# Performance work log

Hardware: AMD Instinct MI355X
Metric: run time of the kernel (lower is better)

The kernel has to match this reference:

```python
import jax, jax.numpy as jnp
import numpy as np

N_NODES = 50000
N_EDGES = 800000
HID = 64


def fake_quant_w(w):
    # symmetric per-tensor int8 fake quantization (num_bits=8)
    s = jnp.maximum(jnp.max(jnp.abs(w)) / 127.0, 1e-8)
    q = jnp.clip(jnp.round(w / s), -127.0, 127.0) * s
    return w + jax.lax.stop_gradient(q - w)


def layer_norm(x, g, b, eps=1e-5):
    mu = jnp.mean(x, axis=-1, keepdims=True)
    var = jnp.var(x, axis=-1, keepdims=True)
    return (x - mu) * jax.lax.rsqrt(var + eps) * g + b


def pointnet_conv(x, pos, src, dst, W, n_nodes):
    # message: cat([x_j, pos_j - pos_i]) @ W_q^T, max-aggregated at i (dst)
    rel = pos[src] - pos[dst]                       # [E, 3]
    feat = jnp.concatenate([x[src], rel], axis=-1)  # [E, C+3]
    msg = feat @ fake_quant_w(W).T                  # [E, 64]
    h = jax.ops.segment_max(msg, dst, num_segments=n_nodes)
    return jnp.where(jnp.isfinite(h), h, 0.0)       # empty segments -> 0


def setup_inputs() -> dict:
    key = jax.random.key(0)
    ks = jax.random.split(key, 16)
    d = {}
    d["x"] = jax.random.normal(ks[0], (N_NODES, 1), jnp.float32)
    d["pos"] = jax.random.normal(ks[1], (N_NODES, 3), jnp.float32)
    d["edge_index"] = jax.random.randint(ks[2], (2, N_EDGES), 0, N_NODES, jnp.int32)
    sc = 0.02
    d["W0"] = jax.random.normal(ks[3], (HID, 1 + 3), jnp.float32) * sc
    d["Ws"] = jax.random.normal(ks[4], (4, HID, HID + 3), jnp.float32) * sc
    d["ln_g"] = jnp.ones((5, HID), jnp.float32)
    d["ln_b"] = jnp.zeros((5, HID), jnp.float32)
    d["mlp_w1"] = jax.random.normal(ks[5], (128, 320), jnp.float32) * sc
    d["mlp_b1"] = jnp.zeros((128,), jnp.float32)
    d["mlp_w2"] = jax.random.normal(ks[6], (128, 128), jnp.float32) * sc
    d["mlp_b2"] = jnp.zeros((128,), jnp.float32)
    d["mlp_w3"] = jax.random.normal(ks[7], (64, 128), jnp.float32) * sc
    d["mlp_b3"] = jnp.zeros((64,), jnp.float32)
    d["mlp_w4"] = jax.random.normal(ks[8], (2, 64), jnp.float32) * sc
    d["mlp_b4"] = jnp.zeros((2,), jnp.float32)
    d["scale"] = jnp.ones((2,), jnp.float32)
    return d


def reference(x, pos, edge_index, W0, Ws, ln_g, ln_b,
              mlp_w1, mlp_b1, mlp_w2, mlp_b2, mlp_w3, mlp_b3, mlp_w4, mlp_b4,
              scale):
    src, dst = edge_index[0], edge_index[1]
    n = x.shape[0]
    embeddings = []
    h = x
    for i in range(5):
        W = W0 if i == 0 else Ws[i - 1]
        h = pointnet_conv(h, pos, src, dst, W, n)
        h = layer_norm(h, ln_g[i], ln_b[i])
        h = jax.nn.relu(h)
        embeddings.append(h)
    z = jnp.concatenate(embeddings, axis=-1)  # [N, 320]
    z = layer_norm(z, jnp.ones((z.shape[-1],), z.dtype), jnp.zeros((z.shape[-1],), z.dtype))
    z = jax.nn.relu(z @ mlp_w1.T + mlp_b1)
    z = jax.nn.relu(z @ mlp_w2.T + mlp_b2)
    z = jax.nn.relu(z @ mlp_w3.T + mlp_b3)
    flow = (z @ mlp_w4.T + mlp_b4) * scale
    return flow
```

## Files before the change

### kernel.cpp

```cpp
#include <hip/hip_runtime.h>
#include <hip/hip_bf16.h>

#define N_NODES 50000
#define N_EDGES 800000
#define NBLK 196

__device__ __forceinline__ float bf2f(unsigned short u) {
    union { unsigned int i; float f; } c; c.i = ((unsigned int)u) << 16; return c.f;
}
__device__ __forceinline__ unsigned short f2bf(float f) {
    union { float f; unsigned int u; } c; c.f = f;
    unsigned int u = c.u;
    u += 0x7fffu + ((u >> 16) & 1u);
    return (unsigned short)(u >> 16);
}
__device__ __forceinline__ float ldin(const void* p, long i, int f32) {
    return f32 ? ((const float*)p)[i] : bf2f(((const unsigned short*)p)[i]);
}
__device__ __forceinline__ float wsum(float v) {
#pragma unroll
    for (int m = 32; m; m >>= 1) v += __shfl_xor(v, m, 64);
    return v;
}

__global__ void probe_kernel(const unsigned short* __restrict__ lng, int* __restrict__ flag) {
    if (threadIdx.x == 0 && blockIdx.x == 0)
        flag[0] = (lng[0] == 0x3F80 && lng[1] == 0x3F80) ? 0 : 1;
}

__global__ __launch_bounds__(256) void hist_kernel(const int* __restrict__ ei, int* __restrict__ deg) {
    int e = blockIdx.x * 256 + threadIdx.x;
    if (e < N_EDGES) atomicAdd(&deg[ei[N_EDGES + e]], 1);
}

__global__ __launch_bounds__(256) void bsum_kernel(const int* __restrict__ deg,
                                                   int* __restrict__ bsum) {
    __shared__ int wt[4];
    const int t = threadIdx.x, lane = t & 63, wid = t >> 6;
    const int i = blockIdx.x * 256 + t;
    int v = (i < N_NODES) ? deg[i] : 0;
    int r = v;
#pragma unroll
    for (int m = 32; m; m >>= 1) r += __shfl_xor(r, m, 64);
    if (lane == 0) wt[wid] = r;
    __syncthreads();
    if (t == 0) bsum[blockIdx.x] = wt[0] + wt[1] + wt[2] + wt[3];
}

__global__ __launch_bounds__(256) void boff_kernel(const int* __restrict__ bsum,
                                                   int* __restrict__ boff) {
    __shared__ int wt[4];
    const int t = threadIdx.x, lane = t & 63, wid = t >> 6;
    int v = (t < NBLK) ? bsum[t] : 0;
    int inc = v;
#pragma unroll
    for (int off = 1; off < 64; off <<= 1) {
        int u = __shfl_up(inc, off, 64);
        if (lane >= off) inc += u;
    }
    if (lane == 63) wt[wid] = inc;
    __syncthreads();
    int woff = 0;
    for (int w = 0; w < wid; ++w) woff += wt[w];
    if (t < NBLK) boff[t] = inc - v + woff;
}

__global__ __launch_bounds__(256) void scanout_kernel(const int* __restrict__ deg,
                                                      const int* __restrict__ boff,
                                                      int* __restrict__ rowptr,
                                                      int* __restrict__ cursor) {
    __shared__ int wt[4];
    const int t = threadIdx.x, lane = t & 63, wid = t >> 6;
    const int i = blockIdx.x * 256 + t;
    int v = (i < N_NODES) ? deg[i] : 0;
    int inc = v;
#pragma unroll
    for (int off = 1; off < 64; off <<= 1) {
        int u = __shfl_up(inc, off, 64);
        if (lane >= off) inc += u;
    }
    if (lane == 63) wt[wid] = inc;
    __syncthreads();
    int woff = 0;
    for (int w = 0; w < wid; ++w) woff += wt[w];
    int excl = inc - v + woff + boff[blockIdx.x];
    if (i < N_NODES) {
        rowptr[i] = excl;
        cursor[i] = excl;
        if (i == N_NODES - 1) rowptr[N_NODES] = excl + v;
    }
}

__global__ __launch_bounds__(256) void scatter_kernel(const int* __restrict__ ei,
                                                      int* __restrict__ cursor,
                                                      int* __restrict__ csr_src) {
    int e = blockIdx.x * 256 + threadIdx.x;
    if (e < N_EDGES) {
        int src = ei[e];
        int dst = ei[N_EDGES + e];
        int p = atomicAdd(&cursor[dst], 1);
        csr_src[p] = src;
    }
}

__global__ __launch_bounds__(256) void quant_kernel(const void* __restrict__ W0,
                                                    const void* __restrict__ Ws,
                                                    float* __restrict__ Wc0,
                                                    float* __restrict__ Wc,
                                                    float* __restrict__ Wr,
                                                    const int* __restrict__ flagp) {
    const int f32 = *flagp;
    int layer = blockIdx.x;
    const void* src = (layer == 0) ? W0 : Ws;
    long sbase = (layer == 0) ? 0 : (long)(layer - 1) * 4288;
    float* dstc = (layer == 0) ? Wc0 : Wc + (size_t)(layer - 1) * 4352;
    float* dstr = (layer == 0) ? nullptr : Wr + (size_t)(layer - 1) * 4352;
    int Ki = (layer == 0) ? 4 : 67;
    int n = 64 * Ki;
    __shared__ float red[256];
    float amax = 0.0f;
    for (int i = threadIdx.x; i < n; i += 256) amax = fmaxf(amax, fabsf(ldin(src, sbase + i, f32)));
    red[threadIdx.x] = amax;
    __syncthreads();
    for (int s = 128; s > 0; s >>= 1) {
        if (threadIdx.x < s) red[threadIdx.x] = fmaxf(red[threadIdx.x], red[threadIdx.x + s]);
        __syncthreads();
    }
    float sc = fmaxf(red[0] / 127.0f, 1e-8f);
    for (int i = threadIdx.x; i < n; i += 256) {
        float w = ldin(src, sbase + i, f32);
        float q = rintf(w / sc);
        q = fminf(fmaxf(q, -127.0f), 127.0f);
        float v = q * sc;
        int o = i / Ki, k = i % Ki;
        dstc[(size_t)k * 64 + o] = v;
        if (dstr) dstr[(size_t)o * 68 + k] = v;
    }
}

__global__ __launch_bounds__(256) void wcvt_kernel(const void* __restrict__ w1,
                                                   const void* __restrict__ w2,
                                                   const void* __restrict__ w3,
                                                   float* __restrict__ Wm,
                                                   const int* __restrict__ flagp) {
    const int f32 = *flagp;
    const int i = blockIdx.x * 256 + threadIdx.x;
    if (i < 40960) Wm[i] = ldin(w1, i, f32);
    else if (i < 57344) Wm[i] = ldin(w2, i - 40960, f32);
    else if (i < 65536) Wm[i] = ldin(w3, i - 57344, f32);
}

__global__ __launch_bounds__(256) void u0_kernel(const void* __restrict__ x,
                                                 const void* __restrict__ pos,
                                                 const float* __restrict__ Wc0,
                                                 float* __restrict__ u,
                                                 const int* __restrict__ flagp) {
    const int f32 = *flagp;
    const int n = blockIdx.x * 256 + threadIdx.x;
    if (n >= N_NODES) return;
    const float xv = ldin(x, n, f32);
    const float p0 = ldin(pos, 3L * n + 0, f32);
    const float p1 = ldin(pos, 3L * n + 1, f32);
    const float p2 = ldin(pos, 3L * n + 2, f32);
    float4* up = reinterpret_cast<float4*>(u + (size_t)n * 64);
#pragma unroll
    for (int q = 0; q < 16; ++q) {
        const float4 w0 = *reinterpret_cast<const float4*>(Wc0 + 0 * 64 + 4 * q);
        const float4 w1 = *reinterpret_cast<const float4*>(Wc0 + 1 * 64 + 4 * q);
        const float4 w2 = *reinterpret_cast<const float4*>(Wc0 + 2 * 64 + 4 * q);
        const float4 w3 = *reinterpret_cast<const float4*>(Wc0 + 3 * 64 + 4 * q);
        float4 o;
        o.x = fmaf(p2, w3.x, fmaf(p1, w2.x, fmaf(p0, w1.x, xv * w0.x)));
        o.y = fmaf(p2, w3.y, fmaf(p1, w2.y, fmaf(p0, w1.y, xv * w0.y)));
        o.z = fmaf(p2, w3.z, fmaf(p1, w2.z, fmaf(p0, w1.z, xv * w0.z)));
        o.w = fmaf(p2, w3.w, fmaf(p1, w2.w, fmaf(p0, w1.w, xv * w0.w)));
        up[q] = o;
    }
}

__global__ __launch_bounds__(256) void agg_kernel(const float* __restrict__ u,
                                                  const void* __restrict__ pos,
                                                  const int* __restrict__ rowptr,
                                                  const int* __restrict__ csr,
                                                  const float* __restrict__ WcV, int vrow,
                                                  const void* __restrict__ lng,
                                                  const void* __restrict__ lnb,
                                                  int lnoff,
                                                  float* __restrict__ z, int out_off,
                                                  const int* __restrict__ flagp) {
    const int f32 = *flagp;
    const int lane = threadIdx.x & 63;
    const int n = __builtin_amdgcn_readfirstlane((blockIdx.x * 256 + threadIdx.x) >> 6);
    if (n >= N_NODES) return;
    const int e0 = rowptr[n], e1 = rowptr[n + 1];
    float acc = -INFINITY;
    int e = e0;
    for (; e + 8 <= e1; e += 8) {
        const float a0 = u[(size_t)csr[e + 0] * 64 + lane];
        const float a1 = u[(size_t)csr[e + 1] * 64 + lane];
        const float a2 = u[(size_t)csr[e + 2] * 64 + lane];
        const float a3 = u[(size_t)csr[e + 3] * 64 + lane];
        const float a4 = u[(size_t)csr[e + 4] * 64 + lane];
        const float a5 = u[(size_t)csr[e + 5] * 64 + lane];
        const float a6 = u[(size_t)csr[e + 6] * 64 + lane];
        const float a7 = u[(size_t)csr[e + 7] * 64 + lane];
        const float m0 = fmaxf(fmaxf(a0, a1), fmaxf(a2, a3));
        const float m1 = fmaxf(fmaxf(a4, a5), fmaxf(a6, a7));
        acc = fmaxf(acc, fmaxf(m0, m1));
    }
    for (; e < e1; ++e)
        acc = fmaxf(acc, u[(size_t)csr[e] * 64 + lane]);
    const float p0 = ldin(pos, 3L * n + 0, f32);
    const float p1 = ldin(pos, 3L * n + 1, f32);
    const float p2 = ldin(pos, 3L * n + 2, f32);
    const float v = fmaf(p2, WcV[(size_t)(vrow + 2) * 64 + lane],
                    fmaf(p1, WcV[(size_t)(vrow + 1) * 64 + lane],
                         p0 * WcV[(size_t)(vrow + 0) * 64 + lane]));
    float h = acc - v;
    if (!isfinite(h)) h = 0.0f;
    const float g = ldin(lng, lnoff + lane, f32);
    const float bb = ldin(lnb, lnoff + lane, f32);
    const float mu = wsum(h) * (1.0f / 64.0f);
    const float dd = h - mu;
    const float var = wsum(dd * dd) * (1.0f / 64.0f);
    float y = dd * rsqrtf(var + 1e-5f) * g + bb;
    y = fmaxf(y, 0.0f);
    z[(size_t)n * 320 + out_off + lane] = y;
}

__global__ __launch_bounds__(256) void un_kernel(const float* __restrict__ z, int in_off,
                                                 const float* __restrict__ Wr,
                                                 const void* __restrict__ pos,
                                                 float* __restrict__ un,
                                                 const int* __restrict__ flagp) {
    __shared__ float At[16][68];
    __shared__ float Wt[16][68];
    const int f32 = *flagp;
    const int tid = threadIdx.x;
    const int bn = blockIdx.x * 64;
    const int o_base = (tid & 15) * 4;
    const int n_base = (tid >> 4) * 4;
    const int sr = tid >> 2;
    const int kq = (tid & 3) * 4;
    float acc[4][4] = {};
    float4 av = make_float4(0.f, 0.f, 0.f, 0.f);
    if (bn + sr < N_NODES)
        av = *reinterpret_cast<const float4*>(z + (size_t)(bn + sr) * 320 + in_off + kq);
    float4 wv = *reinterpret_cast<const float4*>(Wr + (size_t)sr * 68 + kq);
    for (int kk = 0; kk < 64; kk += 16) {
        __syncthreads();
        At[kq + 0][sr] = av.x; At[kq + 1][sr] = av.y; At[kq + 2][sr] = av.z; At[kq + 3][sr] = av.w;
        Wt[kq + 0][sr] = wv.x; Wt[kq + 1][sr] = wv.y; Wt[kq + 2][sr] = wv.z; Wt[kq + 3][sr] = wv.w;
        __syncthreads();
        if (kk + 16 < 64) {
            av = make_float4(0.f, 0.f, 0.f, 0.f);
            if (bn + sr < N_NODES)
                av = *reinterpret_cast<const float4*>(z + (size_t)(bn + sr) * 320 + in_off + kk + 16 + kq);
            wv = *reinterpret_cast<const float4*>(Wr + (size_t)sr * 68 + kk + 16 + kq);
        }
#pragma unroll
        for (int k = 0; k < 16; ++k) {
            const float4 a4 = *reinterpret_cast<const float4*>(&At[k][n_base]);
            const float4 w4 = *reinterpret_cast<const float4*>(&Wt[k][o_base]);
            const float a[4] = { a4.x, a4.y, a4.z, a4.w };
            const float ww[4] = { w4.x, w4.y, w4.z, w4.w };
#pragma unroll
            for (int i = 0; i < 4; ++i)
#pragma unroll
                for (int j = 0; j < 4; ++j)
                    acc[i][j] = fmaf(a[i], ww[j], acc[i][j]);
        }
    }
    float wp[3][4];
#pragma unroll
    for (int c = 0; c < 3; ++c)
#pragma unroll
        for (int j = 0; j < 4; ++j)
            wp[c][j] = Wr[(size_t)(o_base + j) * 68 + 64 + c];
#pragma unroll
    for (int i = 0; i < 4; ++i) {
        const int n = bn + n_base + i;
        if (n < N_NODES) {
            const float p0 = ldin(pos, 3L * n + 0, f32);
            const float p1 = ldin(pos, 3L * n + 1, f32);
            const float p2 = ldin(pos, 3L * n + 2, f32);
#pragma unroll
            for (int j = 0; j < 4; ++j)
                un[(size_t)n * 64 + o_base + j] =
                    fmaf(p2, wp[2][j], fmaf(p1, wp[1][j], fmaf(p0, wp[0][j], acc[i][j])));
        }
    }
}

__global__ __launch_bounds__(256) void lnz_kernel(float* __restrict__ z) {
    const int lane = threadIdx.x & 63;
    const int gw = (blockIdx.x * blockDim.x + threadIdx.x) >> 6;
    const int nw = (gridDim.x * blockDim.x) >> 6;
    for (int nidx = gw; nidx < N_NODES; nidx += nw) {
        float v[5];
        float s = 0.f;
#pragma unroll
        for (int j = 0; j < 5; ++j) {
            v[j] = z[(size_t)nidx * 320 + j * 64 + lane];
            s += v[j];
        }
        float mu = wsum(s) * (1.0f / 320.0f);
        float q = 0.f;
#pragma unroll
        for (int j = 0; j < 5; ++j) { float d = v[j] - mu; q = fmaf(d, d, q); }
        float var = wsum(q) * (1.0f / 320.0f);
        float rs = rsqrtf(var + 1e-5f);
#pragma unroll
        for (int j = 0; j < 5; ++j) z[(size_t)nidx * 320 + j * 64 + lane] = (v[j] - mu) * rs;
    }
}

__global__ __launch_bounds__(256) void gemm_kernel(const float* __restrict__ A,
                                                   const float* __restrict__ W,
                                                   const void* __restrict__ bias,
                                                   float* __restrict__ C,
                                                   int Ki, int Ko,
                                                   const int* __restrict__ flagp) {
    __shared__ float At[16][68];
    __shared__ float Wt[16][68];
    const int f32 = *flagp;
    const int tid = threadIdx.x;
    const int bn = blockIdx.x * 64;
    const int bo = blockIdx.y * 64;
    const int o_base = (tid & 15) * 4;
    const int n_base = (tid >> 4) * 4;
    const int sr = tid >> 2;
    const int kq = (tid & 3) * 4;
    float acc[4][4] = {};
    float4 av = make_float4(0.f, 0.f, 0.f, 0.f);
    if (bn + sr < N_NODES)
        av = *reinterpret_cast<const float4*>(A + (size_t)(bn + sr) * Ki + kq);
    float4 wv = *reinterpret_cast<const float4*>(W + (size_t)(bo + sr) * Ki + kq);
    for (int kk = 0; kk < Ki; kk += 16) {
        __syncthreads();
        At[kq + 0][sr] = av.x; At[kq + 1][sr] = av.y; At[kq + 2][sr] = av.z; At[kq + 3][sr] = av.w;
        Wt[kq + 0][sr] = wv.x; Wt[kq + 1][sr] = wv.y; Wt[kq + 2][sr] = wv.z; Wt[kq + 3][sr] = wv.w;
        __syncthreads();
        if (kk + 16 < Ki) {
            av = make_float4(0.f, 0.f, 0.f, 0.f);
            if (bn + sr < N_NODES)
                av = *reinterpret_cast<const float4*>(A + (size_t)(bn + sr) * Ki + kk + 16 + kq);
            wv = *reinterpret_cast<const float4*>(W + (size_t)(bo + sr) * Ki + kk + 16 + kq);
        }
#pragma unroll
        for (int k = 0; k < 16; ++k) {
            const float4 a4 = *reinterpret_cast<const float4*>(&At[k][n_base]);
            const float4 w4 = *reinterpret_cast<const float4*>(&Wt[k][o_base]);
            const float a[4] = { a4.x, a4.y, a4.z, a4.w };
            const float ww[4] = { w4.x, w4.y, w4.z, w4.w };
#pragma unroll
            for (int i = 0; i < 4; ++i)
#pragma unroll
                for (int j = 0; j < 4; ++j)
                    acc[i][j] = fmaf(a[i], ww[j], acc[i][j]);
        }
    }
    float bj[4];
#pragma unroll
    for (int j = 0; j < 4; ++j) bj[j] = ldin(bias, bo + o_base + j, f32);
#pragma unroll
    for (int i = 0; i < 4; ++i) {
        int n = bn + n_base + i;
        if (n < N_NODES) {
#pragma unroll
            for (int j = 0; j < 4; ++j) {
                float c = fmaxf(acc[i][j] + bj[j], 0.0f);
                C[(size_t)n * Ko + bo + o_base + j] = c;
            }
        }
    }
}

__global__ __launch_bounds__(256) void out_kernel(const float* __restrict__ h3,
                                                  const void* __restrict__ w4,
                                                  const void* __restrict__ b4,
                                                  const void* __restrict__ scale,
                                                  void* __restrict__ out,
                                                  const int* __restrict__ flagp) {
    const int f32 = *flagp;
    const int lane = threadIdx.x & 63;
    const int gw = (blockIdx.x * blockDim.x + threadIdx.x) >> 6;
    const int nw = (gridDim.x * blockDim.x) >> 6;
    const float wa = ldin(w4, lane, f32);
    const float wb = ldin(w4, 64 + lane, f32);
    const float b0 = ldin(b4, 0, f32), b1 = ldin(b4, 1, f32);
    const float s0 = ldin(scale, 0, f32), s1 = ldin(scale, 1, f32);
    for (int nidx = gw; nidx < N_NODES; nidx += nw) {
        float h = h3[(size_t)nidx * 64 + lane];
        float d0 = wsum(h * wa);
        float d1 = wsum(h * wb);
        if (lane == 0) {
            float o0 = (d0 + b0) * s0;
            float o1 = (d1 + b1) * s1;
            if (f32) {
                ((float*)out)[nidx * 2 + 0] = o0;
                ((float*)out)[nidx * 2 + 1] = o1;
            } else {
                ((unsigned short*)out)[nidx * 2 + 0] = f2bf(o0);
                ((unsigned short*)out)[nidx * 2 + 1] = f2bf(o1);
            }
        }
    }
}

extern "C" void kernel_launch(void* const* d_in, const int* in_sizes, int n_in,
                              void* d_out, int out_size, void* d_ws, size_t ws_size,
                              hipStream_t stream) {
    (void)in_sizes; (void)n_in; (void)out_size; (void)ws_size;
    const void* x    = d_in[0];
    const void* pos  = d_in[1];
    const int*  ei   = (const int*)d_in[2];
    const void* W0   = d_in[3];
    const void* Ws   = d_in[4];
    const void* lng  = d_in[5];
    const void* lnb  = d_in[6];
    const void* w1   = d_in[7];
    const void* b1   = d_in[8];
    const void* w2   = d_in[9];
    const void* b2   = d_in[10];
    const void* w3   = d_in[11];
    const void* b3   = d_in[12];
    const void* w4   = d_in[13];
    const void* b4   = d_in[14];
    const void* scl  = d_in[15];

    float* z      = (float*)d_ws;
    float* h1     = z + 16000000;
    float* Wc0    = h1 + 6400000;
    float* Wc     = Wc0 + 256;
    float* Wr     = Wc + 17408;
    float* Wm     = Wr + 17408;
    int*   deg    = (int*)(Wm + 65536);
    int*   rowptr = deg + N_NODES;
    int*   cursor = rowptr + (N_NODES + 1);
    int*   flag   = cursor + N_NODES;
    int*   csr    = flag + 1;
    int*   bsum   = csr + N_EDGES;
    int*   boff   = bsum + 256;
    float* Wm1 = Wm, *Wm2 = Wm + 40960, *Wm3 = Wm + 57344;
    float* ua     = h1;
    float* ub     = h1 + 3200000;
    float* h2 = z;
    float* h3 = z + 6400000;

    hipMemsetAsync(deg, 0, N_NODES * sizeof(int), stream);
    probe_kernel<<<1, 64, 0, stream>>>((const unsigned short*)lng, flag);
    hist_kernel<<<(N_EDGES + 255) / 256, 256, 0, stream>>>(ei, deg);
    bsum_kernel<<<NBLK, 256, 0, stream>>>(deg, bsum);
    boff_kernel<<<1, 256, 0, stream>>>(bsum, boff);
    scanout_kernel<<<NBLK, 256, 0, stream>>>(deg, boff, rowptr, cursor);
    scatter_kernel<<<(N_EDGES + 255) / 256, 256, 0, stream>>>(ei, cursor, csr);
    quant_kernel<<<5, 256, 0, stream>>>(W0, Ws, Wc0, Wc, Wr, flag);
    wcvt_kernel<<<256, 256, 0, stream>>>(w1, w2, w3, Wm, flag);

    const int gagg = (N_NODES * 64 + 255) / 256;
    const int gun  = (N_NODES + 63) / 64;

    u0_kernel<<<NBLK, 256, 0, stream>>>(x, pos, Wc0, ua, flag);
    agg_kernel<<<gagg, 256, 0, stream>>>(ua, pos, rowptr, csr, Wc0, 1,
                                         lng, lnb, 0, z, 0, flag);
    un_kernel<<<gun, 256, 0, stream>>>(z, 0, Wr + 0 * 4352, pos, ub, flag);
    agg_kernel<<<gagg, 256, 0, stream>>>(ub, pos, rowptr, csr, Wc + 0 * 4352, 64,
                                         lng, lnb, 64, z, 64, flag);
    un_kernel<<<gun, 256, 0, stream>>>(z, 64, Wr + 1 * 4352, pos, ua, flag);
    agg_kernel<<<gagg, 256, 0, stream>>>(ua, pos, rowptr, csr, Wc + 1 * 4352, 64,
                                         lng, lnb, 128, z, 128, flag);
    un_kernel<<<gun, 256, 0, stream>>>(z, 128, Wr + 2 * 4352, pos, ub, flag);
    agg_kernel<<<gagg, 256, 0, stream>>>(ub, pos, rowptr, csr, Wc + 2 * 4352, 64,
                                         lng, lnb, 192, z, 192, flag);
    un_kernel<<<gun, 256, 0, stream>>>(z, 192, Wr + 3 * 4352, pos, ua, flag);
    agg_kernel<<<gagg, 256, 0, stream>>>(ua, pos, rowptr, csr, Wc + 3 * 4352, 64,
                                         lng, lnb, 256, z, 256, flag);

    lnz_kernel<<<512, 256, 0, stream>>>(z);

    dim3 g1((N_NODES + 63) / 64, 2);
    gemm_kernel<<<g1, 256, 0, stream>>>(z, Wm1, b1, h1, 320, 128, flag);
    dim3 g2((N_NODES + 63) / 64, 2);
    gemm_kernel<<<g2, 256, 0, stream>>>(h1, Wm2, b2, h2, 128, 128, flag);
    dim3 g3((N_NODES + 63) / 64, 1);
    gemm_kernel<<<g3, 256, 0, stream>>>(h2, Wm3, b3, h3, 128, 64, flag);
    out_kernel<<<512, 256, 0, stream>>>(h3, w4, b4, scl, d_out, flag);
}
```

Measured before the change: 586.0 us.

## Fuse final layernorm into last agg and GEMM, merge output head into GEMM3

The last aggregation kernel now also computes per-node mean and rstd over the full 320-wide embedding and writes them to a stats buffer. The first MLP GEMM applies that normalization while staging A into shared memory, which removes the separate lnz pass that read and rewrote z. The 128-output GEMMs now cover all 128 outputs per block (8 per thread) instead of using two grid columns, so A is read once. The third GEMM keeps its tile in LDS and computes the final 2-wide head directly, dropping the h3 round trip and out_kernel. The agg gather loop is also widened to 16-way unrolling with a 4-way tail, which raises register pressure.

```diff
diff --git a/kernel.cpp b/kernel.cpp
--- a/kernel.cpp
+++ b/kernel.cpp
@@ -187,6 +187,7 @@
                                                   const void* __restrict__ lnb,
                                                   int lnoff,
                                                   float* __restrict__ z, int out_off,
+                                                  float2* __restrict__ stats,
                                                   const int* __restrict__ flagp) {
     const int f32 = *flagp;
     const int lane = threadIdx.x & 63;
@@ -195,18 +196,35 @@
     const int e0 = rowptr[n], e1 = rowptr[n + 1];
     float acc = -INFINITY;
     int e = e0;
-    for (; e + 8 <= e1; e += 8) {
-        const float a0 = u[(size_t)csr[e + 0] * 64 + lane];
-        const float a1 = u[(size_t)csr[e + 1] * 64 + lane];
-        const float a2 = u[(size_t)csr[e + 2] * 64 + lane];
-        const float a3 = u[(size_t)csr[e + 3] * 64 + lane];
-        const float a4 = u[(size_t)csr[e + 4] * 64 + lane];
-        const float a5 = u[(size_t)csr[e + 5] * 64 + lane];
-        const float a6 = u[(size_t)csr[e + 6] * 64 + lane];
-        const float a7 = u[(size_t)csr[e + 7] * 64 + lane];
-        const float m0 = fmaxf(fmaxf(a0, a1), fmaxf(a2, a3));
-        const float m1 = fmaxf(fmaxf(a4, a5), fmaxf(a6, a7));
-        acc = fmaxf(acc, fmaxf(m0, m1));
+    for (; e + 16 <= e1; e += 16) {
+        float t0 = u[(size_t)csr[e + 0] * 64 + lane];
+        float t1 = u[(size_t)csr[e + 1] * 64 + lane];
+        float t2 = u[(size_t)csr[e + 2] * 64 + lane];
+        float t3 = u[(size_t)csr[e + 3] * 64 + lane];
+        float t4 = u[(size_t)csr[e + 4] * 64 + lane];
+        float t5 = u[(size_t)csr[e + 5] * 64 + lane];
+        float t6 = u[(size_t)csr[e + 6] * 64 + lane];
+        float t7 = u[(size_t)csr[e + 7] * 64 + lane];
+        float t8 = u[(size_t)csr[e + 8] * 64 + lane];
+        float t9 = u[(size_t)csr[e + 9] * 64 + lane];
+        float ta = u[(size_t)csr[e + 10] * 64 + lane];
+        float tb = u[(size_t)csr[e + 11] * 64 + lane];
+        float tc = u[(size_t)csr[e + 12] * 64 + lane];
+        float td = u[(size_t)csr[e + 13] * 64 + lane];
+        float te = u[(size_t)csr[e + 14] * 64 + lane];
+        float tf = u[(size_t)csr[e + 15] * 64 + lane];
+        float m0 = fmaxf(fmaxf(t0, t1), fmaxf(t2, t3));
+        float m1 = fmaxf(fmaxf(t4, t5), fmaxf(t6, t7));
+        float m2 = fmaxf(fmaxf(t8, t9), fmaxf(ta, tb));
+        float m3 = fmaxf(fmaxf(tc, td), fmaxf(te, tf));
+        acc = fmaxf(acc, fmaxf(fmaxf(m0, m1), fmaxf(m2, m3)));
+    }
+    for (; e + 4 <= e1; e += 4) {
+        float t0 = u[(size_t)csr[e + 0] * 64 + lane];
+        float t1 = u[(size_t)csr[e + 1] * 64 + lane];
+        float t2 = u[(size_t)csr[e + 2] * 64 + lane];
+        float t3 = u[(size_t)csr[e + 3] * 64 + lane];
+        acc = fmaxf(acc, fmaxf(fmaxf(t0, t1), fmaxf(t2, t3)));
     }
     for (; e < e1; ++e)
         acc = fmaxf(acc, u[(size_t)csr[e] * 64 + lane]);
@@ -226,6 +244,22 @@
     float y = dd * rsqrtf(var + 1e-5f) * g + bb;
     y = fmaxf(y, 0.0f);
     z[(size_t)n * 320 + out_off + lane] = y;
+    if (stats) {
+        const float* zr = z + (size_t)n * 320;
+        const float v0 = zr[0 * 64 + lane];
+        const float v1 = zr[1 * 64 + lane];
+        const float v2 = zr[2 * 64 + lane];
+        const float v3 = zr[3 * 64 + lane];
+        const float s = ((v0 + v1) + (v2 + v3)) + y;
+        const float mu2 = wsum(s) * (1.0f / 320.0f);
+        float q = (v0 - mu2) * (v0 - mu2);
+        q = fmaf(v1 - mu2, v1 - mu2, q);
+        q = fmaf(v2 - mu2, v2 - mu2, q);
+        q = fmaf(v3 - mu2, v3 - mu2, q);
+        q = fmaf(y - mu2, y - mu2, q);
+        const float var2 = wsum(q) * (1.0f / 320.0f);
+        if (lane == 0) stats[n] = make_float2(mu2, rsqrtf(var2 + 1e-5f));
+    }
 }
 
 __global__ __launch_bounds__(256) void un_kernel(const float* __restrict__ z, int in_off,
@@ -292,41 +326,97 @@
     }
 }
 
-__global__ __launch_bounds__(256) void lnz_kernel(float* __restrict__ z) {
-    const int lane = threadIdx.x & 63;
-    const int gw = (blockIdx.x * blockDim.x + threadIdx.x) >> 6;
-    const int nw = (gridDim.x * blockDim.x) >> 6;
-    for (int nidx = gw; nidx < N_NODES; nidx += nw) {
-        float v[5];
-        float s = 0.f;
-#pragma unroll
-        for (int j = 0; j < 5; ++j) {
-            v[j] = z[(size_t)nidx * 320 + j * 64 + lane];
-            s += v[j];
-        }
-        float mu = wsum(s) * (1.0f / 320.0f);
-        float q = 0.f;
-#pragma unroll
-        for (int j = 0; j < 5; ++j) { float d = v[j] - mu; q = fmaf(d, d, q); }
-        float var = wsum(q) * (1.0f / 320.0f);
-        float rs = rsqrtf(var + 1e-5f);
-#pragma unroll
-        for (int j = 0; j < 5; ++j) z[(size_t)nidx * 320 + j * 64 + lane] = (v[j] - mu) * rs;
-    }
-}
-
-__global__ __launch_bounds__(256) void gemm_kernel(const float* __restrict__ A,
-                                                   const float* __restrict__ W,
-                                                   const void* __restrict__ bias,
-                                                   float* __restrict__ C,
-                                                   int Ki, int Ko,
-                                                   const int* __restrict__ flagp) {
+__global__ __launch_bounds__(256) void gemm128_kernel(const float* __restrict__ A,
+                                                      const float* __restrict__ W,
+                                                      const void* __restrict__ bias,
+                                                      const float2* __restrict__ stats,
+                                                      float* __restrict__ C,
+                                                      int Ki,
+                                                      const int* __restrict__ flagp) {
+    __shared__ float At[16][68];
+    __shared__ float Wt[16][132];
+    const int f32 = *flagp;
+    const int tid = threadIdx.x;
+    const int bn = blockIdx.x * 64;
+    const int sr = tid >> 2;
+    const int kq = (tid & 3) * 4;
+    const int wr = tid >> 1;
+    const int kq2 = (tid & 1) * 8;
+    const int n_base = (tid >> 4) * 4;
+    const int o_base = (tid & 15) * 8;
+    float mu = 0.f, rs = 1.f;
+    if (stats && bn + sr < N_NODES) { float2 st = stats[bn + sr]; mu = st.x; rs = st.y; }
+    float acc[4][8] = {};
+    float4 av = make_float4(0.f, 0.f, 0.f, 0.f);
+    if (bn + sr < N_NODES)
+        av = *reinterpret_cast<const float4*>(A + (size_t)(bn + sr) * Ki + kq);
+    float4 wv0 = *reinterpret_cast<const float4*>(W + (size_t)wr * Ki + kq2);
+    float4 wv1 = *reinterpret_cast<const float4*>(W + (size_t)wr * Ki + kq2 + 4);
+    for (int kk = 0; kk < Ki; kk += 16) {
+        __syncthreads();
+        At[kq + 0][sr] = (av.x - mu) * rs;
+        At[kq + 1][sr] = (av.y - mu) * rs;
+        At[kq + 2][sr] = (av.z - mu) * rs;
+        At[kq + 3][sr] = (av.w - mu) * rs;
+        Wt[kq2 + 0][wr] = wv0.x; Wt[kq2 + 1][wr] = wv0.y;
+        Wt[kq2 + 2][wr] = wv0.z; Wt[kq2 + 3][wr] = wv0.w;
+        Wt[kq2 + 4][wr] = wv1.x; Wt[kq2 + 5][wr] = wv1.y;
+        Wt[kq2 + 6][wr] = wv1.z; Wt[kq2 + 7][wr] = wv1.w;
+        __syncthreads();
+        if (kk + 16 < Ki) {
+            av = make_float4(0.f, 0.f, 0.f, 0.f);
+            if (bn + sr < N_NODES)
+                av = *reinterpret_cast<const float4*>(A + (size_t)(bn + sr) * Ki + kk + 16 + kq);
+            wv0 = *reinterpret_cast<const float4*>(W + (size_t)wr * Ki + kk + 16 + kq2);
+            wv1 = *reinterpret_cast<const float4*>(W + (size_t)wr * Ki + kk + 16 + kq2 + 4);
+        }
+#pragma unroll
+        for (int k = 0; k < 16; ++k) {
+            const float4 a4 = *reinterpret_cast<const float4*>(&At[k][n_base]);
+            const float4 wa = *reinterpret_cast<const float4*>(&Wt[k][o_base]);
+            const float4 wb = *reinterpret_cast<const float4*>(&Wt[k][o_base + 4]);
+            const float a[4] = { a4.x, a4.y, a4.z, a4.w };
+            const float ww[8] = { wa.x, wa.y, wa.z, wa.w, wb.x, wb.y, wb.z, wb.w };
+#pragma unroll
+            for (int i = 0; i < 4; ++i)
+#pragma unroll
+                for (int j = 0; j < 8; ++j)
+                    acc[i][j] = fmaf(a[i], ww[j], acc[i][j]);
+        }
+    }
+    float bj[8];
+#pragma unroll
+    for (int j = 0; j < 8; ++j) bj[j] = ldin(bias, o_base + j, f32);
+#pragma unroll
+    for (int i = 0; i < 4; ++i) {
+        const int n = bn + n_base + i;
+        if (n < N_NODES) {
+            float4 c0, c1;
+            c0.x = fmaxf(acc[i][0] + bj[0], 0.f); c0.y = fmaxf(acc[i][1] + bj[1], 0.f);
+            c0.z = fmaxf(acc[i][2] + bj[2], 0.f); c0.w = fmaxf(acc[i][3] + bj[3], 0.f);
+            c1.x = fmaxf(acc[i][4] + bj[4], 0.f); c1.y = fmaxf(acc[i][5] + bj[5], 0.f);
+            c1.z = fmaxf(acc[i][6] + bj[6], 0.f); c1.w = fmaxf(acc[i][7] + bj[7], 0.f);
+            *reinterpret_cast<float4*>(C + (size_t)n * 128 + o_base) = c0;
+            *reinterpret_cast<float4*>(C + (size_t)n * 128 + o_base + 4) = c1;
+        }
+    }
+}
+
+__global__ __launch_bounds__(256) void gemm64out_kernel(const float* __restrict__ A,
+                                                        const float* __restrict__ W,
+                                                        const void* __restrict__ bias,
+                                                        const void* __restrict__ w4,
+                                                        const void* __restrict__ b4,
+                                                        const void* __restrict__ scale,
+                                                        void* __restrict__ out,
+                                                        const int* __restrict__ flagp) {
     __shared__ float At[16][68];
     __shared__ float Wt[16][68];
+    __shared__ float h3t[64][65];
     const int f32 = *flagp;
     const int tid = threadIdx.x;
     const int bn = blockIdx.x * 64;
-    const int bo = blockIdx.y * 64;
+    const int Ki = 128;
     const int o_base = (tid & 15) * 4;
     const int n_base = (tid >> 4) * 4;
     const int sr = tid >> 2;
@@ -335,7 +425,7 @@
     float4 av = make_float4(0.f, 0.f, 0.f, 0.f);
     if (bn + sr < N_NODES)
         av = *reinterpret_cast<const float4*>(A + (size_t)(bn + sr) * Ki + kq);
-    float4 wv = *reinterpret_cast<const float4*>(W + (size_t)(bo + sr) * Ki + kq);
+    float4 wv = *reinterpret_cast<const float4*>(W + (size_t)sr * Ki + kq);
     for (int kk = 0; kk < Ki; kk += 16) {
         __syncthreads();
         At[kq + 0][sr] = av.x; At[kq + 1][sr] = av.y; At[kq + 2][sr] = av.z; At[kq + 3][sr] = av.w;
@@ -345,14 +435,14 @@
             av = make_float4(0.f, 0.f, 0.f, 0.f);
             if (bn + sr < N_NODES)
                 av = *reinterpret_cast<const float4*>(A + (size_t)(bn + sr) * Ki + kk + 16 + kq);
-            wv = *reinterpret_cast<const float4*>(W + (size_t)(bo + sr) * Ki + kk + 16 + kq);
+            wv = *reinterpret_cast<const float4*>(W + (size_t)sr * Ki + kk + 16 + kq);
         }
 #pragma unroll
         for (int k = 0; k < 16; ++k) {
             const float4 a4 = *reinterpret_cast<const float4*>(&At[k][n_base]);
-            const float4 w4 = *reinterpret_cast<const float4*>(&Wt[k][o_base]);
+            const float4 w4v = *reinterpret_cast<const float4*>(&Wt[k][o_base]);
             const float a[4] = { a4.x, a4.y, a4.z, a4.w };
-            const float ww[4] = { w4.x, w4.y, w4.z, w4.w };
+            const float ww[4] = { w4v.x, w4v.y, w4v.z, w4v.w };
 #pragma unroll
             for (int i = 0; i < 4; ++i)
 #pragma unroll
@@ -362,47 +452,35 @@
     }
     float bj[4];
 #pragma unroll
-    for (int j = 0; j < 4; ++j) bj[j] = ldin(bias, bo + o_base + j, f32);
-#pragma unroll
-    for (int i = 0; i < 4; ++i) {
-        int n = bn + n_base + i;
-        if (n < N_NODES) {
-#pragma unroll
-            for (int j = 0; j < 4; ++j) {
-                float c = fmaxf(acc[i][j] + bj[j], 0.0f);
-                C[(size_t)n * Ko + bo + o_base + j] = c;
-            }
-        }
-    }
-}
-
-__global__ __launch_bounds__(256) void out_kernel(const float* __restrict__ h3,
-                                                  const void* __restrict__ w4,
-                                                  const void* __restrict__ b4,
-                                                  const void* __restrict__ scale,
-                                                  void* __restrict__ out,
-                                                  const int* __restrict__ flagp) {
-    const int f32 = *flagp;
-    const int lane = threadIdx.x & 63;
-    const int gw = (blockIdx.x * blockDim.x + threadIdx.x) >> 6;
-    const int nw = (gridDim.x * blockDim.x) >> 6;
+    for (int j = 0; j < 4; ++j) bj[j] = ldin(bias, o_base + j, f32);
+    __syncthreads();
+#pragma unroll
+    for (int i = 0; i < 4; ++i)
+#pragma unroll
+        for (int j = 0; j < 4; ++j)
+            h3t[n_base + i][o_base + j] = fmaxf(acc[i][j] + bj[j], 0.f);
+    __syncthreads();
+    const int lane = tid & 63, wid = tid >> 6;
     const float wa = ldin(w4, lane, f32);
     const float wb = ldin(w4, 64 + lane, f32);
     const float b0 = ldin(b4, 0, f32), b1 = ldin(b4, 1, f32);
     const float s0 = ldin(scale, 0, f32), s1 = ldin(scale, 1, f32);
-    for (int nidx = gw; nidx < N_NODES; nidx += nw) {
-        float h = h3[(size_t)nidx * 64 + lane];
-        float d0 = wsum(h * wa);
-        float d1 = wsum(h * wb);
+#pragma unroll
+    for (int r = wid * 16; r < wid * 16 + 16; ++r) {
+        const int n = bn + r;
+        if (n >= N_NODES) break;
+        const float hv = h3t[r][lane];
+        const float d0 = wsum(hv * wa);
+        const float d1 = wsum(hv * wb);
         if (lane == 0) {
-            float o0 = (d0 + b0) * s0;
-            float o1 = (d1 + b1) * s1;
+            const float o0 = (d0 + b0) * s0;
+            const float o1 = (d1 + b1) * s1;
             if (f32) {
-                ((float*)out)[nidx * 2 + 0] = o0;
-                ((float*)out)[nidx * 2 + 1] = o1;
+                ((float*)out)[n * 2 + 0] = o0;
+                ((float*)out)[n * 2 + 1] = o1;
             } else {
-                ((unsigned short*)out)[nidx * 2 + 0] = f2bf(o0);
-                ((unsigned short*)out)[nidx * 2 + 1] = f2bf(o1);
+                ((unsigned short*)out)[n * 2 + 0] = f2bf(o0);
+                ((unsigned short*)out)[n * 2 + 1] = f2bf(o1);
             }
         }
     }
@@ -442,11 +520,11 @@
     int*   csr    = flag + 1;
     int*   bsum   = csr + N_EDGES;
     int*   boff   = bsum + 256;
+    float2* stats = (float2*)(boff + 256);
     float* Wm1 = Wm, *Wm2 = Wm + 40960, *Wm3 = Wm + 57344;
     float* ua     = h1;
     float* ub     = h1 + 3200000;
     float* h2 = z;
-    float* h3 = z + 6400000;
 
     hipMemsetAsync(deg, 0, N_NODES * sizeof(int), stream);
     probe_kernel<<<1, 64, 0, stream>>>((const unsigned short*)lng, flag);
@@ -463,27 +541,22 @@
 
     u0_kernel<<<NBLK, 256, 0, stream>>>(x, pos, Wc0, ua, flag);
     agg_kernel<<<gagg, 256, 0, stream>>>(ua, pos, rowptr, csr, Wc0, 1,
-                                         lng, lnb, 0, z, 0, flag);
+                                         lng, lnb, 0, z, 0, nullptr, flag);
     un_kernel<<<gun, 256, 0, stream>>>(z, 0, Wr + 0 * 4352, pos, ub, flag);
     agg_kernel<<<gagg, 256, 0, stream>>>(ub, pos, rowptr, csr, Wc + 0 * 4352, 64,
-                                         lng, lnb, 64, z, 64, flag);
+                                         lng, lnb, 64, z, 64, nullptr, flag);
     un_kernel<<<gun, 256, 0, stream>>>(z, 64, Wr + 1 * 4352, pos, ua, flag);
     agg_kernel<<<gagg, 256, 0, stream>>>(ua, pos, rowptr, csr, Wc + 1 * 4352, 64,
-                                         lng, lnb, 128, z, 128, flag);
+                                         lng, lnb, 128, z, 128, nullptr, flag);
     un_kernel<<<gun, 256, 0, stream>>>(z, 128, Wr + 2 * 4352, pos, ub, flag);
     agg_kernel<<<gagg, 256, 0, stream>>>(ub, pos, rowptr, csr, Wc + 2 * 4352, 64,
-                                         lng, lnb, 192, z, 192, flag);
+                                         lng, lnb, 192, z, 192, nullptr, flag);
     un_kernel<<<gun, 256, 0, stream>>>(z, 192, Wr + 3 * 4352, pos, ua, flag);
     agg_kernel<<<gagg, 256, 0, stream>>>(ua, pos, rowptr, csr, Wc + 3 * 4352, 64,
-                                         lng, lnb, 256, z, 256, flag);
-
-    lnz_kernel<<<512, 256, 0, stream>>>(z);
-
-    dim3 g1((N_NODES + 63) / 64, 2);
-    gemm_kernel<<<g1, 256, 0, stream>>>(z, Wm1, b1, h1, 320, 128, flag);
-    dim3 g2((N_NODES + 63) / 64, 2);
-    gemm_kernel<<<g2, 256, 0, stream>>>(h1, Wm2, b2, h2, 128, 128, flag);
-    dim3 g3((N_NODES + 63) / 64, 1);
-    gemm_kernel<<<g3, 256, 0, stream>>>(h2, Wm3, b3, h3, 128, 64, flag);
-    out_kernel<<<512, 256, 0, stream>>>(h3, w4, b4, scl, d_out, flag);
-}
+                                         lng, lnb, 256, z, 256, stats, flag);
+
+    const int gg = (N_NODES + 63) / 64;
+    gemm128_kernel<<<gg, 256, 0, stream>>>(z, Wm1, b1, stats, h1, 320, flag);
+    gemm128_kernel<<<gg, 256, 0, stream>>>(h1, Wm2, b2, nullptr, h2, 128, flag);
+    gemm64out_kernel<<<gg, 256, 0, stream>>>(h2, Wm3, b3, w4, b4, scl, d_out, flag);
+}
```

New measurement: 571.3 us. 1.03x faster.
